# Kernel optimization log

Hardware: AMD Instinct MI355X
Metric: run time of the kernel (lower is better)

## Reference

```python
import jax, jax.numpy as jnp
import numpy as np

N = 100000
E = 1600000
D = 64  # in = hidden = out channels


def setup_inputs() -> dict:
    key = jax.random.key(0)
    ks = jax.random.split(key, 6)
    x = jax.random.normal(ks[0], (N, D), dtype=jnp.float32)
    edge_index = jax.random.randint(ks[1], (2, E), 0, N, dtype=jnp.int64)
    # bias-free linear weights, torch Linear layout [out, in]
    s = 1.0 / np.sqrt(D)
    W0 = jax.random.uniform(ks[2], (D, D), jnp.float32, -s, s)
    W1 = jax.random.uniform(ks[3], (D, D), jnp.float32, -s, s)
    Wm = jax.random.uniform(ks[4], (D, D), jnp.float32, -s, s)
    eps0 = jnp.zeros((), jnp.float32)  # train_eps=True, init 0.0
    eps1 = jnp.zeros((), jnp.float32)
    return {"x": x, "edge_index": edge_index, "W0": W0, "eps0": eps0,
            "W1": W1, "eps1": eps1, "Wm": Wm}


def reference(x, edge_index, W0, eps0, W1, eps1, Wm):
    n = x.shape[0]
    src, dst = edge_index[0], edge_index[1]

    def gin_conv(h, W, eps):
        # sparse adjacency sum-aggregation: out[i] = sum_{j->i} h[j]
        agg = jax.ops.segment_sum(h[src], dst, num_segments=n)
        # eps-scaled self-loop + bias-free linear
        return (agg + (1.0 + eps) * h) @ W.T

    h1 = jax.nn.relu(gin_conv(x, W0, eps0))   # xs[0], [N, D]
    h2 = jax.nn.relu(gin_conv(h1, W1, eps1))  # xs[1], [N, D]
    return (h1 @ Wm.T + h2) / 2.0
```

## Files before the change

### kernel.cpp

```cpp
#include <hip/hip_runtime.h>
#include <hip/hip_fp16.h>


__global__ __launch_bounds__(256) void zero_convert_kernel(
    int* __restrict__ deg, int n,
    const float* __restrict__ in, __half* __restrict__ outh, int total4)
{
    int i = blockIdx.x * blockDim.x + threadIdx.x;
    int stride = gridDim.x * blockDim.x;
    for (int k = i; k < n; k += stride) deg[k] = 0;
    const float4* in4 = (const float4*)in;
    uint2* out4 = (uint2*)outh;
    for (int k = i; k < total4; k += stride) {
        float4 v = in4[k];
        __half2 a = __floats2half2_rn(v.x, v.y);
        __half2 b = __floats2half2_rn(v.z, v.w);
        uint2 u;
        u.x = __builtin_bit_cast(unsigned int, a);
        u.y = __builtin_bit_cast(unsigned int, b);
        out4[k] = u;
    }
}

__global__ __launch_bounds__(256) void zero_int_kernel(int* __restrict__ p, int n)
{
    int i = blockIdx.x * blockDim.x + threadIdx.x;
    int stride = gridDim.x * blockDim.x;
    for (; i < n; i += stride) p[i] = 0;
}

__global__ __launch_bounds__(256) void hist_rank_kernel(
    const int* __restrict__ dst, int* __restrict__ deg,
    int* __restrict__ rank, int E)
{
    int base = (blockIdx.x * blockDim.x + threadIdx.x) * 16;
    if (base + 15 < E) {
        int4 a = *(const int4*)&dst[base];
        int4 b = *(const int4*)&dst[base + 4];
        int4 c = *(const int4*)&dst[base + 8];
        int4 d = *(const int4*)&dst[base + 12];
        int r0 = atomicAdd(&deg[a.x], 1);
        int r1 = atomicAdd(&deg[a.y], 1);
        int r2 = atomicAdd(&deg[a.z], 1);
        int r3 = atomicAdd(&deg[a.w], 1);
        int r4 = atomicAdd(&deg[b.x], 1);
        int r5 = atomicAdd(&deg[b.y], 1);
        int r6 = atomicAdd(&deg[b.z], 1);
        int r7 = atomicAdd(&deg[b.w], 1);
        int r8 = atomicAdd(&deg[c.x], 1);
        int r9 = atomicAdd(&deg[c.y], 1);
        int rA = atomicAdd(&deg[c.z], 1);
        int rB = atomicAdd(&deg[c.w], 1);
        int rC = atomicAdd(&deg[d.x], 1);
        int rD = atomicAdd(&deg[d.y], 1);
        int rE = atomicAdd(&deg[d.z], 1);
        int rF = atomicAdd(&deg[d.w], 1);
        *(int4*)&rank[base]      = make_int4(r0, r1, r2, r3);
        *(int4*)&rank[base + 4]  = make_int4(r4, r5, r6, r7);
        *(int4*)&rank[base + 8]  = make_int4(r8, r9, rA, rB);
        *(int4*)&rank[base + 12] = make_int4(rC, rD, rE, rF);
    } else {
        for (int e = base; e < E; ++e) rank[e] = atomicAdd(&deg[dst[e]], 1);
    }
}

__global__ __launch_bounds__(256) void hist_kernel(
    const int* __restrict__ dst, int* __restrict__ deg, int E)
{
    int e4 = (blockIdx.x * blockDim.x + threadIdx.x) * 4;
    if (e4 + 3 < E) {
        int4 d = *(const int4*)&dst[e4];
        atomicAdd(&deg[d.x], 1);
        atomicAdd(&deg[d.y], 1);
        atomicAdd(&deg[d.z], 1);
        atomicAdd(&deg[d.w], 1);
    } else {
        for (int e = e4; e < E; ++e) atomicAdd(&deg[dst[e]], 1);
    }
}

__global__ __launch_bounds__(256) void scanA_kernel(
    const int* __restrict__ deg, int* __restrict__ off,
    int* __restrict__ bsum, int n)
{
    __shared__ int tmp[256];
    int t = threadIdx.x;
    int base = blockIdx.x * 1024 + t * 4;
    int v0 = 0, v1 = 0, v2 = 0, v3 = 0;
    if (base + 3 < n) {
        int4 q = *(const int4*)&deg[base];
        v0 = q.x; v1 = q.y; v2 = q.z; v3 = q.w;
    } else {
        if (base + 0 < n) v0 = deg[base + 0];
        if (base + 1 < n) v1 = deg[base + 1];
        if (base + 2 < n) v2 = deg[base + 2];
    }
    int tot = v0 + v1 + v2 + v3;
    tmp[t] = tot;
    __syncthreads();
    for (int d = 1; d < 256; d <<= 1) {
        int x = (t >= d) ? tmp[t - d] : 0;
        __syncthreads();
        tmp[t] += x;
        __syncthreads();
    }
    int incl = tmp[t];
    int p = incl - tot;
    if (base + 0 < n) off[base + 0] = p;
    if (base + 1 < n) off[base + 1] = p + v0;
    if (base + 2 < n) off[base + 2] = p + v0 + v1;
    if (base + 3 < n) off[base + 3] = p + v0 + v1 + v2;
    if (t == 255) bsum[blockIdx.x] = incl;
}

__global__ __launch_bounds__(256) void scanB_kernel(int* __restrict__ bsum, int nb)
{
    __shared__ int tmp[256];
    int t = threadIdx.x;
    int v = (t < nb) ? bsum[t] : 0;
    tmp[t] = v;
    __syncthreads();
    for (int d = 1; d < 256; d <<= 1) {
        int x = (t >= d) ? tmp[t - d] : 0;
        __syncthreads();
        tmp[t] += x;
        __syncthreads();
    }
    if (t < nb) bsum[t] = tmp[t] - v;
}

__global__ __launch_bounds__(256) void scanC_kernel(
    int* __restrict__ off, int* __restrict__ cursor,
    const int* __restrict__ bsum, int n, int E)
{
    int t = threadIdx.x;
    int add = bsum[blockIdx.x];
    int base = blockIdx.x * 1024 + t * 4;
#pragma unroll
    for (int q = 0; q < 4; ++q) {
        int idx = base + q;
        if (idx < n) {
            int v = off[idx] + add;
            off[idx] = v;
            if (cursor) cursor[idx] = v;
        }
    }
    if (blockIdx.x == 0 && t == 0) off[n] = E;
}

__global__ __launch_bounds__(256) void fill_rank_kernel(
    const int* __restrict__ src, const int* __restrict__ dst,
    const int* __restrict__ rank, const int* __restrict__ off,
    int* __restrict__ bucket, int E)
{
    int base = (blockIdx.x * blockDim.x + threadIdx.x) * 8;
    if (base + 7 < E) {
        int4 d0 = *(const int4*)&dst[base];
        int4 d1 = *(const int4*)&dst[base + 4];
        int4 r0 = *(const int4*)&rank[base];
        int4 r1 = *(const int4*)&rank[base + 4];
        int4 s0 = *(const int4*)&src[base];
        int4 s1 = *(const int4*)&src[base + 4];
        bucket[off[d0.x] + r0.x] = s0.x;
        bucket[off[d0.y] + r0.y] = s0.y;
        bucket[off[d0.z] + r0.z] = s0.z;
        bucket[off[d0.w] + r0.w] = s0.w;
        bucket[off[d1.x] + r1.x] = s1.x;
        bucket[off[d1.y] + r1.y] = s1.y;
        bucket[off[d1.z] + r1.z] = s1.z;
        bucket[off[d1.w] + r1.w] = s1.w;
    } else {
        for (int e = base; e < E; ++e) bucket[off[dst[e]] + rank[e]] = src[e];
    }
}

__global__ __launch_bounds__(256) void fill_kernel(
    const int* __restrict__ src, const int* __restrict__ dst,
    int* __restrict__ cursor, int* __restrict__ bucket, int E)
{
    int e = blockIdx.x * blockDim.x + threadIdx.x;
    if (e < E) {
        int d = dst[e];
        int p = atomicAdd(&cursor[d], 1);
        bucket[p] = src[e];
    }
}

#define WPB 8

__device__ __forceinline__ __half2 bc_h2(unsigned int u)
{
    return __builtin_bit_cast(__half2, u);
}
__device__ __forceinline__ unsigned int bc_u(__half2 h)
{
    return __builtin_bit_cast(unsigned int, h);
}

#if __has_builtin(__builtin_amdgcn_fdot2)
typedef _Float16 half2_v __attribute__((ext_vector_type(2)));
__device__ __forceinline__ float fdot2(unsigned int a, unsigned int b, float c)
{
    return __builtin_amdgcn_fdot2(__builtin_bit_cast(half2_v, a),
                                  __builtin_bit_cast(half2_v, b), c, false);
}
#else
__device__ __forceinline__ float fdot2(unsigned int a, unsigned int b, float c)
{
    float2 af = __half22float2(bc_h2(a));
    float2 bf = __half22float2(bc_h2(b));
    return fmaf(af.x, bf.x, fmaf(af.y, bf.y, c));
}
#endif


__device__ __forceinline__ void xreduce4(__half2& a0, __half2& a1,
                                         __half2& a2, __half2& a3)
{
#pragma unroll
    for (int mask = 8; mask <= 32; mask <<= 1) {
        a0 = __hadd2(a0, bc_h2((unsigned int)__shfl_xor((int)bc_u(a0), mask, 64)));
        a1 = __hadd2(a1, bc_h2((unsigned int)__shfl_xor((int)bc_u(a1), mask, 64)));
        a2 = __hadd2(a2, bc_h2((unsigned int)__shfl_xor((int)bc_u(a2), mask, 64)));
        a3 = __hadd2(a3, bc_h2((unsigned int)__shfl_xor((int)bc_u(a3), mask, 64)));
    }
}

__device__ __forceinline__ void gather8(
    const __half* __restrict__ hh, const int* __restrict__ bucket,
    int beg, int end, int g, int l8,
    __half2& a0, __half2& a1, __half2& a2, __half2& a3)
{
    int j = beg;
    for (; j + 16 <= end; j += 16) {
        int sa = bucket[j + g];
        int sb = bucket[j + 8 + g];
        uint4 va = *(const uint4*)&hh[(size_t)sa * 64 + l8 * 8];
        uint4 vb = *(const uint4*)&hh[(size_t)sb * 64 + l8 * 8];
        a0 = __hadd2(__hadd2(a0, bc_h2(va.x)), bc_h2(vb.x));
        a1 = __hadd2(__hadd2(a1, bc_h2(va.y)), bc_h2(vb.y));
        a2 = __hadd2(__hadd2(a2, bc_h2(va.z)), bc_h2(vb.z));
        a3 = __hadd2(__hadd2(a3, bc_h2(va.w)), bc_h2(vb.w));
    }
    if (j + 8 <= end) {
        int sa = bucket[j + g];
        uint4 va = *(const uint4*)&hh[(size_t)sa * 64 + l8 * 8];
        a0 = __hadd2(a0, bc_h2(va.x));
        a1 = __hadd2(a1, bc_h2(va.y));
        a2 = __hadd2(a2, bc_h2(va.z));
        a3 = __hadd2(a3, bc_h2(va.w));
        j += 8;
    }
    if (j < end) {
        int jj = j + g;
        int sc = bucket[(jj < end) ? jj : (end - 1)];
        __half2 m2 = __float2half2_rn((jj < end) ? 1.0f : 0.0f);
        uint4 vc = *(const uint4*)&hh[(size_t)sc * 64 + l8 * 8];
        a0 = __hfma2(bc_h2(vc.x), m2, a0);
        a1 = __hfma2(bc_h2(vc.y), m2, a1);
        a2 = __hfma2(bc_h2(vc.z), m2, a2);
        a3 = __hfma2(bc_h2(vc.w), m2, a3);
    }
}

__global__ __launch_bounds__(512) void fused_gin_h_kernel(
    const __half* __restrict__ hh, const int* __restrict__ off,
    const int* __restrict__ bucket, const float* __restrict__ W,
    const float* __restrict__ eps, __half* __restrict__ outh, int n)
{
    __shared__ __half WhS[4096];
    __shared__ __half rowh[WPB][64];
    int tid = threadIdx.x;
    for (int idx = tid; idx < 4096; idx += 512) {
        int row = idx >> 6, col = idx & 63;
        WhS[(col >> 3) * 512 + row * 8 + (col & 7)] = __float2half(W[idx]);
    }
    __syncthreads();
    float s = 1.0f + eps[0];
    __half2 s2 = __float2half2_rn(s);
    int lane = tid & 63;
    int w = tid >> 6;
    int l8 = lane & 7;
    int g = lane >> 3;
    int wavesTotal = gridDim.x * WPB;
    const uint4* Wh4 = (const uint4*)WhS;
    for (int i = blockIdx.x * WPB + w; i < n; i += wavesTotal) {
        int2 be = *(const int2*)&off[i];
        int beg = __builtin_amdgcn_readfirstlane(be.x);
        int end = __builtin_amdgcn_readfirstlane(be.y);
        __half2 a0 = bc_h2(0u), a1 = bc_h2(0u), a2 = bc_h2(0u), a3 = bc_h2(0u);
        gather8(hh, bucket, beg, end, g, l8, a0, a1, a2, a3);
        xreduce4(a0, a1, a2, a3);
        if (g == 0) {
            uint4 sv = *(const uint4*)&hh[(size_t)i * 64 + l8 * 8];
            a0 = __hfma2(bc_h2(sv.x), s2, a0);
            a1 = __hfma2(bc_h2(sv.y), s2, a1);
            a2 = __hfma2(bc_h2(sv.z), s2, a2);
            a3 = __hfma2(bc_h2(sv.w), s2, a3);
            uint4 st;
            st.x = bc_u(a0); st.y = bc_u(a1); st.z = bc_u(a2); st.w = bc_u(a3);
            *(uint4*)&rowh[w][l8 * 8] = st;
        }
        __builtin_amdgcn_wave_barrier();
        float o = 0.f;
#pragma unroll
        for (int k4 = 0; k4 < 8; ++k4) {
            uint4 wv = Wh4[k4 * 64 + lane];
            uint4 rv = *(const uint4*)&rowh[w][k4 * 8];
            o = fdot2(wv.x, rv.x, o);
            o = fdot2(wv.y, rv.y, o);
            o = fdot2(wv.z, rv.z, o);
            o = fdot2(wv.w, rv.w, o);
        }
        outh[(size_t)i * 64 + lane] = __float2half(fmaxf(o, 0.f));
        __builtin_amdgcn_wave_barrier();
    }
}

__global__ __launch_bounds__(512) void fused_final_h_kernel(
    const __half* __restrict__ hh1, const int* __restrict__ off,
    const int* __restrict__ bucket, const float* __restrict__ W1,
    const float* __restrict__ Wm, const float* __restrict__ eps,
    float* __restrict__ out, int n)
{
    __shared__ __half W1hS[4096];
    __shared__ __half WmhS[4096];
    __shared__ __half rowh[WPB][64];
    __shared__ __half selfh[WPB][64];
    int tid = threadIdx.x;
    for (int idx = tid; idx < 4096; idx += 512) {
        int row = idx >> 6, col = idx & 63;
        int li = (col >> 3) * 512 + row * 8 + (col & 7);
        W1hS[li] = __float2half(W1[idx]);
        WmhS[li] = __float2half(Wm[idx]);
    }
    __syncthreads();
    float s = 1.0f + eps[0];
    __half2 s2 = __float2half2_rn(s);
    int lane = tid & 63;
    int w = tid >> 6;
    int l8 = lane & 7;
    int g = lane >> 3;
    int wavesTotal = gridDim.x * WPB;
    const uint4* W1h4 = (const uint4*)W1hS;
    const uint4* Wmh4 = (const uint4*)WmhS;
    for (int i = blockIdx.x * WPB + w; i < n; i += wavesTotal) {
        int2 be = *(const int2*)&off[i];
        int beg = __builtin_amdgcn_readfirstlane(be.x);
        int end = __builtin_amdgcn_readfirstlane(be.y);
        __half2 a0 = bc_h2(0u), a1 = bc_h2(0u), a2 = bc_h2(0u), a3 = bc_h2(0u);
        gather8(hh1, bucket, beg, end, g, l8, a0, a1, a2, a3);
        xreduce4(a0, a1, a2, a3);
        if (g == 0) {
            uint4 sv = *(const uint4*)&hh1[(size_t)i * 64 + l8 * 8];
            *(uint4*)&selfh[w][l8 * 8] = sv;
            a0 = __hfma2(bc_h2(sv.x), s2, a0);
            a1 = __hfma2(bc_h2(sv.y), s2, a1);
            a2 = __hfma2(bc_h2(sv.z), s2, a2);
            a3 = __hfma2(bc_h2(sv.w), s2, a3);
            uint4 st;
            st.x = bc_u(a0); st.y = bc_u(a1); st.z = bc_u(a2); st.w = bc_u(a3);
            *(uint4*)&rowh[w][l8 * 8] = st;
        }
        __builtin_amdgcn_wave_barrier();
        float o1 = 0.f, o2 = 0.f;
#pragma unroll
        for (int k4 = 0; k4 < 8; ++k4) {
            uint4 wv1 = W1h4[k4 * 64 + lane];
            uint4 wv2 = Wmh4[k4 * 64 + lane];
            uint4 rv  = *(const uint4*)&rowh[w][k4 * 8];
            uint4 sv  = *(const uint4*)&selfh[w][k4 * 8];
            o1 = fdot2(wv1.x, rv.x, o1);
            o1 = fdot2(wv1.y, rv.y, o1);
            o1 = fdot2(wv1.z, rv.z, o1);
            o1 = fdot2(wv1.w, rv.w, o1);
            o2 = fdot2(wv2.x, sv.x, o2);
            o2 = fdot2(wv2.y, sv.y, o2);
            o2 = fdot2(wv2.z, sv.z, o2);
            o2 = fdot2(wv2.w, sv.w, o2);
        }
        out[(size_t)i * 64 + lane] = (fmaxf(o1, 0.f) + o2) * 0.5f;
        __builtin_amdgcn_wave_barrier();
    }
}

__device__ __forceinline__ float dot4(float4 a, float4 b)
{
    return a.x * b.x + a.y * b.y + a.z * b.z + a.w * b.w;
}

__device__ __forceinline__ float4 gather_row_f32(
    const float* __restrict__ h, const int* __restrict__ bucket,
    int beg, int end, int g, int l16, float4 acc4)
{
    int j = beg;
    for (; j + 8 <= end; j += 8) {
        int sa = bucket[j + g];
        int sb = bucket[j + 4 + g];
        float4 va = *(const float4*)&h[(size_t)sa * 64 + l16 * 4];
        float4 vb = *(const float4*)&h[(size_t)sb * 64 + l16 * 4];
        acc4.x += va.x + vb.x;
        acc4.y += va.y + vb.y;
        acc4.z += va.z + vb.z;
        acc4.w += va.w + vb.w;
    }
    if (j + 4 <= end) {
        int sa = bucket[j + g];
        float4 va = *(const float4*)&h[(size_t)sa * 64 + l16 * 4];
        acc4.x += va.x; acc4.y += va.y; acc4.z += va.z; acc4.w += va.w;
        j += 4;
    }
    if (j < end) {
        int jj = j + g;
        int sc = bucket[(jj < end) ? jj : (end - 1)];
        float m = (jj < end) ? 1.0f : 0.0f;
        float4 vc = *(const float4*)&h[(size_t)sc * 64 + l16 * 4];
        acc4.x = fmaf(vc.x, m, acc4.x);
        acc4.y = fmaf(vc.y, m, acc4.y);
        acc4.z = fmaf(vc.z, m, acc4.z);
        acc4.w = fmaf(vc.w, m, acc4.w);
    }
    return acc4;
}

__global__ __launch_bounds__(512) void fused_gin_kernel(
    const float* __restrict__ h, const int* __restrict__ off,
    const int* __restrict__ bucket, const float* __restrict__ W,
    const float* __restrict__ eps, float* __restrict__ out, int n)
{
    __shared__ float Ws[64][68];
    __shared__ float P[WPB][4][64];
    __shared__ float rowbuf[WPB][64];
    int tid = threadIdx.x;
    for (int idx = tid; idx < 4096; idx += 512) Ws[idx >> 6][idx & 63] = W[idx];
    __syncthreads();
    float s = 1.0f + eps[0];
    int lane = tid & 63;
    int w = tid >> 6;
    int l16 = lane & 15;
    int g = lane >> 4;
    int wavesTotal = gridDim.x * WPB;
    for (int i = blockIdx.x * WPB + w; i < n; i += wavesTotal) {
        float4 init = make_float4(0.f, 0.f, 0.f, 0.f);
        if (g == 0) {
            float4 self4 = *(const float4*)&h[(size_t)i * 64 + l16 * 4];
            init = make_float4(s * self4.x, s * self4.y, s * self4.z, s * self4.w);
        }
        int2 be = *(const int2*)&off[i];
        int beg = __builtin_amdgcn_readfirstlane(be.x);
        int end = __builtin_amdgcn_readfirstlane(be.y);
        float4 acc4 = gather_row_f32(h, bucket, beg, end, g, l16, init);
        *(float4*)&P[w][g][l16 * 4] = acc4;
        __builtin_amdgcn_wave_barrier();
        float r0 = P[w][0][lane], r1 = P[w][1][lane];
        float r2 = P[w][2][lane], r3 = P[w][3][lane];
        rowbuf[w][lane] = (r0 + r1) + (r2 + r3);
        __builtin_amdgcn_wave_barrier();
        const float4* wrow = (const float4*)&Ws[lane][0];
        const float4* rrow = (const float4*)&rowbuf[w][0];
        float o = 0.f;
#pragma unroll
        for (int k4 = 0; k4 < 16; ++k4) o += dot4(wrow[k4], rrow[k4]);
        out[(size_t)i * 64 + lane] = fmaxf(o, 0.f);
        __builtin_amdgcn_wave_barrier();
    }
}

__global__ __launch_bounds__(512) void fused_final_csr_kernel(
    const float* __restrict__ h1, const int* __restrict__ off,
    const int* __restrict__ bucket, const float* __restrict__ W1,
    const float* __restrict__ Wm, const float* __restrict__ eps,
    float* __restrict__ out, int n)
{
    __shared__ float W1s[64][68];
    __shared__ float Wms[64][68];
    __shared__ float P[WPB][4][64];
    __shared__ float rowbuf[WPB][64];
    __shared__ float selfbuf[WPB][64];
    int tid = threadIdx.x;
    for (int idx = tid; idx < 4096; idx += 512) {
        W1s[idx >> 6][idx & 63] = W1[idx];
        Wms[idx >> 6][idx & 63] = Wm[idx];
    }
    __syncthreads();
    float s = 1.0f + eps[0];
    int lane = tid & 63;
    int w = tid >> 6;
    int l16 = lane & 15;
    int g = lane >> 4;
    int wavesTotal = gridDim.x * WPB;
    for (int i = blockIdx.x * WPB + w; i < n; i += wavesTotal) {
        float4 init = make_float4(0.f, 0.f, 0.f, 0.f);
        if (g == 0) {
            float4 self4 = *(const float4*)&h1[(size_t)i * 64 + l16 * 4];
            *(float4*)&selfbuf[w][l16 * 4] = self4;
            init = make_float4(s * self4.x, s * self4.y, s * self4.z, s * self4.w);
        }
        int2 be = *(const int2*)&off[i];
        int beg = __builtin_amdgcn_readfirstlane(be.x);
        int end = __builtin_amdgcn_readfirstlane(be.y);
        float4 acc4 = gather_row_f32(h1, bucket, beg, end, g, l16, init);
        *(float4*)&P[w][g][l16 * 4] = acc4;
        __builtin_amdgcn_wave_barrier();
        float r0 = P[w][0][lane], r1 = P[w][1][lane];
        float r2 = P[w][2][lane], r3 = P[w][3][lane];
        rowbuf[w][lane] = (r0 + r1) + (r2 + r3);
        __builtin_amdgcn_wave_barrier();
        const float4* w1row = (const float4*)&W1s[lane][0];
        const float4* wmrow = (const float4*)&Wms[lane][0];
        const float4* rrow  = (const float4*)&rowbuf[w][0];
        const float4* srow  = (const float4*)&selfbuf[w][0];
        float o1 = 0.f, o2 = 0.f;
#pragma unroll
        for (int k4 = 0; k4 < 16; ++k4) {
            o1 += dot4(w1row[k4], rrow[k4]);
            o2 += dot4(wmrow[k4], srow[k4]);
        }
        out[(size_t)i * 64 + lane] = (fmaxf(o1, 0.f) + o2) * 0.5f;
        __builtin_amdgcn_wave_barrier();
    }
}

__global__ __launch_bounds__(256) void init_scale_kernel(
    const float* __restrict__ h, const float* __restrict__ eps,
    float* __restrict__ agg, int total4)
{
    float s = 1.0f + eps[0];
    int i = blockIdx.x * blockDim.x + threadIdx.x;
    int stride = gridDim.x * blockDim.x;
    const float4* h4 = (const float4*)h;
    float4* a4 = (float4*)agg;
    for (; i < total4; i += stride) {
        float4 v = h4[i];
        v.x *= s; v.y *= s; v.z *= s; v.w *= s;
        a4[i] = v;
    }
}

__global__ __launch_bounds__(256) void scatter_kernel(
    const float* __restrict__ h, const int* __restrict__ src,
    const int* __restrict__ dst, float* __restrict__ agg, int E)
{
    int lane = threadIdx.x & 63;
    int e = blockIdx.x * 4 + (threadIdx.x >> 6);
    if (e >= E) return;
    int s = src[e];
    int d = dst[e];
    atomicAdd(&agg[(size_t)d * 64 + lane], h[(size_t)s * 64 + lane]);
}

__global__ __launch_bounds__(256) void gemm_relu_kernel(
    const float* __restrict__ A, const float* __restrict__ W,
    float* __restrict__ out, int n)
{
    __shared__ float Wt[64][65];
    __shared__ float rowbuf[4][64];
    int tid = threadIdx.x;
    for (int i = tid; i < 4096; i += 256) Wt[i & 63][i >> 6] = W[i];
    __syncthreads();
    int lane = tid & 63;
    int w = tid >> 6;
    int wavesTotal = gridDim.x * 4;
    for (int i = blockIdx.x * 4 + w; i < n; i += wavesTotal) {
        rowbuf[w][lane] = A[(size_t)i * 64 + lane];
        __builtin_amdgcn_wave_barrier();
        float o = 0.f;
#pragma unroll
        for (int k = 0; k < 64; ++k) o += rowbuf[w][k] * Wt[k][lane];
        out[(size_t)i * 64 + lane] = fmaxf(o, 0.f);
        __builtin_amdgcn_wave_barrier();
    }
}

__global__ __launch_bounds__(256) void final_kernel(
    const float* __restrict__ Agg, const float* __restrict__ H1,
    const float* __restrict__ W1, const float* __restrict__ Wm,
    float* __restrict__ out, int n)
{
    __shared__ float W1t[64][65];
    __shared__ float Wmt[64][65];
    __shared__ float rowbuf[4][64];
    __shared__ float selfbuf[4][64];
    int tid = threadIdx.x;
    for (int i = tid; i < 4096; i += 256) {
        W1t[i & 63][i >> 6] = W1[i];
        Wmt[i & 63][i >> 6] = Wm[i];
    }
    __syncthreads();
    int lane = tid & 63;
    int w = tid >> 6;
    int wavesTotal = gridDim.x * 4;
    for (int i = blockIdx.x * 4 + w; i < n; i += wavesTotal) {
        rowbuf[w][lane] = Agg[(size_t)i * 64 + lane];
        selfbuf[w][lane] = H1[(size_t)i * 64 + lane];
        __builtin_amdgcn_wave_barrier();
        float o1 = 0.f, o2 = 0.f;
#pragma unroll
        for (int k = 0; k < 64; ++k) {
            o1 += rowbuf[w][k] * W1t[k][lane];
            o2 += selfbuf[w][k] * Wmt[k][lane];
        }
        out[(size_t)i * 64 + lane] = (fmaxf(o1, 0.f) + o2) * 0.5f;
        __builtin_amdgcn_wave_barrier();
    }
}

extern "C" void kernel_launch(void* const* d_in, const int* in_sizes, int n_in,
                              void* d_out, int out_size, void* d_ws, size_t ws_size,
                              hipStream_t stream)
{
    const float* x    = (const float*)d_in[0];
    const int*   ei   = (const int*)d_in[1];
    const float* W0   = (const float*)d_in[2];
    const float* eps0 = (const float*)d_in[3];
    const float* W1   = (const float*)d_in[4];
    const float* eps1 = (const float*)d_in[5];
    const float* Wm   = (const float*)d_in[6];
    float* out = (float*)d_out;

    int n = in_sizes[0] / 64;
    int E = in_sizes[1] / 2;
    const int* src = ei;
    const int* dst = ei + E;

    auto align1k = [](size_t v) { return (v + 1023) & ~(size_t)1023; };

    size_t hhx_off    = 0;
    size_t hh1_off    = align1k(hhx_off + (size_t)n * 64 * 2);
    size_t off_off    = align1k(hh1_off + (size_t)n * 64 * 2);
    size_t deg_off    = align1k(off_off + (size_t)(n + 1) * 4);
    size_t bsum_off   = align1k(deg_off + (size_t)n * 4);
    size_t bucket_off = align1k(bsum_off + 256 * 4);
    size_t rank_off   = align1k(bucket_off + (size_t)(E + 64) * 4);
    size_t need_A2    = rank_off + (size_t)E * 4;

    size_t b_h1_off     = 0;
    size_t b_off_off    = align1k(b_h1_off + (size_t)n * 64 * 4);
    size_t b_deg_off    = align1k(b_off_off + (size_t)(n + 1) * 4);
    size_t b_cursor_off = align1k(b_deg_off + (size_t)n * 4);
    size_t b_bsum_off   = align1k(b_cursor_off + (size_t)n * 4);
    size_t b_bucket_off = align1k(b_bsum_off + 256 * 4);
    size_t need_B       = b_bucket_off + (size_t)E * 4;

    int nb = (n + 1023) / 1024;
    int e8Blocks  = (E + 2047) / 2048;
    int e16Blocks = (E + 4095) / 4096;
    int total4 = n * 16;

    if (ws_size >= need_A2) {
        __half* hhx  = (__half*)((char*)d_ws + hhx_off);
        __half* hh1  = (__half*)((char*)d_ws + hh1_off);
        int* off     = (int*)((char*)d_ws + off_off);
        int* deg     = (int*)((char*)d_ws + deg_off);
        int* bsum    = (int*)((char*)d_ws + bsum_off);
        int* bucket  = (int*)((char*)d_ws + bucket_off);
        int* rank    = (int*)((char*)d_ws + rank_off);

        zero_convert_kernel<<<2048, 256, 0, stream>>>(deg, n, x, hhx, total4);
        hist_rank_kernel<<<e16Blocks, 256, 0, stream>>>(dst, deg, rank, E);
        scanA_kernel<<<nb, 256, 0, stream>>>(deg, off, bsum, n);
        scanB_kernel<<<1, 256, 0, stream>>>(bsum, nb);
        scanC_kernel<<<nb, 256, 0, stream>>>(off, (int*)nullptr, bsum, n, E);
        fill_rank_kernel<<<e8Blocks, 256, 0, stream>>>(src, dst, rank, off, bucket, E);

        fused_gin_h_kernel<<<2048, 512, 0, stream>>>(hhx, off, bucket, W0, eps0, hh1, n);
        fused_final_h_kernel<<<2048, 512, 0, stream>>>(hh1, off, bucket, W1, Wm, eps1, out, n);
    } else if (ws_size >= need_B) {
        float* h1    = (float*)((char*)d_ws + b_h1_off);
        int* off     = (int*)((char*)d_ws + b_off_off);
        int* deg     = (int*)((char*)d_ws + b_deg_off);
        int* cursor  = (int*)((char*)d_ws + b_cursor_off);
        int* bsum    = (int*)((char*)d_ws + b_bsum_off);
        int* bucket  = (int*)((char*)d_ws + b_bucket_off);

        zero_int_kernel<<<256, 256, 0, stream>>>(deg, n);
        hist_kernel<<<(E + 1023) / 1024, 256, 0, stream>>>(dst, deg, E);
        scanA_kernel<<<nb, 256, 0, stream>>>(deg, off, bsum, n);
        scanB_kernel<<<1, 256, 0, stream>>>(bsum, nb);
        scanC_kernel<<<nb, 256, 0, stream>>>(off, cursor, bsum, n, E);
        fill_kernel<<<(E + 255) / 256, 256, 0, stream>>>(src, dst, cursor, bucket, E);

        fused_gin_kernel<<<1024, 512, 0, stream>>>(x, off, bucket, W0, eps0, h1, n);
        fused_final_csr_kernel<<<768, 512, 0, stream>>>(h1, off, bucket, W1, Wm, eps1, out, n);
    } else {
        float* agg = (float*)d_ws;
        float* h1  = out;
        int scatterBlocks = (E + 3) / 4;

        init_scale_kernel<<<2048, 256, 0, stream>>>(x, eps0, agg, total4);
        scatter_kernel<<<scatterBlocks, 256, 0, stream>>>(x, src, dst, agg, E);
        gemm_relu_kernel<<<2048, 256, 0, stream>>>(agg, W0, h1, n);
        init_scale_kernel<<<2048, 256, 0, stream>>>(h1, eps1, agg, total4);
        scatter_kernel<<<scatterBlocks, 256, 0, stream>>>(h1, src, dst, agg, E);
        final_kernel<<<2048, 256, 0, stream>>>(agg, h1, W1, Wm, out, n);
    }
}
```

Baseline: 219.8 us.

## Partition degree histogram into 8 copies and store edge ranks as 16-bit

The degree histogram is split into 8 per-partition count arrays, chosen by block index, so the atomics on popular destinations are spread across copies. A per-node pass turns the partition counts into per-partition prefix offsets, and a second pass adds the global CSR offset. Ranks are stored as 16-bit values to halve that traffic. The cost is two extra node-level kernels, more memory to zero, and an assumption that no per-partition degree exceeds 65535.

```diff
diff --git a/kernel.cpp b/kernel.cpp
--- a/kernel.cpp
+++ b/kernel.cpp
@@ -2,13 +2,17 @@
 #include <hip/hip_fp16.h>
 
 
+#define HIST_EPT 16
+#define HIST_EPB 4096
+#define NPART 8
+
 __global__ __launch_bounds__(256) void zero_convert_kernel(
-    int* __restrict__ deg, int n,
+    int* __restrict__ cnt, int cntTotal,
     const float* __restrict__ in, __half* __restrict__ outh, int total4)
 {
     int i = blockIdx.x * blockDim.x + threadIdx.x;
     int stride = gridDim.x * blockDim.x;
-    for (int k = i; k < n; k += stride) deg[k] = 0;
+    for (int k = i; k < cntTotal; k += stride) cnt[k] = 0;
     const float4* in4 = (const float4*)in;
     uint2* out4 = (uint2*)outh;
     for (int k = i; k < total4; k += stride) {
@@ -29,54 +33,75 @@
     for (; i < n; i += stride) p[i] = 0;
 }
 
-__global__ __launch_bounds__(256) void hist_rank_kernel(
-    const int* __restrict__ dst, int* __restrict__ deg,
-    int* __restrict__ rank, int E)
-{
-    int base = (blockIdx.x * blockDim.x + threadIdx.x) * 16;
-    if (base + 15 < E) {
+__global__ __launch_bounds__(256) void hist_rank_part_kernel(
+    const int* __restrict__ dst, int* __restrict__ cnt,
+    unsigned short* __restrict__ rank16, int E, int n)
+{
+    int b = blockIdx.x;
+    int* cp = cnt + (size_t)(b & (NPART - 1)) * n;
+    int base = b * HIST_EPB + threadIdx.x * HIST_EPT;
+    if (base + HIST_EPT - 1 < E) {
         int4 a = *(const int4*)&dst[base];
-        int4 b = *(const int4*)&dst[base + 4];
+        int4 bb = *(const int4*)&dst[base + 4];
         int4 c = *(const int4*)&dst[base + 8];
         int4 d = *(const int4*)&dst[base + 12];
-        int r0 = atomicAdd(&deg[a.x], 1);
-        int r1 = atomicAdd(&deg[a.y], 1);
-        int r2 = atomicAdd(&deg[a.z], 1);
-        int r3 = atomicAdd(&deg[a.w], 1);
-        int r4 = atomicAdd(&deg[b.x], 1);
-        int r5 = atomicAdd(&deg[b.y], 1);
-        int r6 = atomicAdd(&deg[b.z], 1);
-        int r7 = atomicAdd(&deg[b.w], 1);
-        int r8 = atomicAdd(&deg[c.x], 1);
-        int r9 = atomicAdd(&deg[c.y], 1);
-        int rA = atomicAdd(&deg[c.z], 1);
-        int rB = atomicAdd(&deg[c.w], 1);
-        int rC = atomicAdd(&deg[d.x], 1);
-        int rD = atomicAdd(&deg[d.y], 1);
-        int rE = atomicAdd(&deg[d.z], 1);
-        int rF = atomicAdd(&deg[d.w], 1);
-        *(int4*)&rank[base]      = make_int4(r0, r1, r2, r3);
-        *(int4*)&rank[base + 4]  = make_int4(r4, r5, r6, r7);
-        *(int4*)&rank[base + 8]  = make_int4(r8, r9, rA, rB);
-        *(int4*)&rank[base + 12] = make_int4(rC, rD, rE, rF);
+        unsigned int r0 = (unsigned int)atomicAdd(&cp[a.x], 1);
+        unsigned int r1 = (unsigned int)atomicAdd(&cp[a.y], 1);
+        unsigned int r2 = (unsigned int)atomicAdd(&cp[a.z], 1);
+        unsigned int r3 = (unsigned int)atomicAdd(&cp[a.w], 1);
+        unsigned int r4 = (unsigned int)atomicAdd(&cp[bb.x], 1);
+        unsigned int r5 = (unsigned int)atomicAdd(&cp[bb.y], 1);
+        unsigned int r6 = (unsigned int)atomicAdd(&cp[bb.z], 1);
+        unsigned int r7 = (unsigned int)atomicAdd(&cp[bb.w], 1);
+        unsigned int r8 = (unsigned int)atomicAdd(&cp[c.x], 1);
+        unsigned int r9 = (unsigned int)atomicAdd(&cp[c.y], 1);
+        unsigned int rA = (unsigned int)atomicAdd(&cp[c.z], 1);
+        unsigned int rB = (unsigned int)atomicAdd(&cp[c.w], 1);
+        unsigned int rC = (unsigned int)atomicAdd(&cp[d.x], 1);
+        unsigned int rD = (unsigned int)atomicAdd(&cp[d.y], 1);
+        unsigned int rE = (unsigned int)atomicAdd(&cp[d.z], 1);
+        unsigned int rF = (unsigned int)atomicAdd(&cp[d.w], 1);
+        uint4 w0, w1;
+        w0.x = (r1 << 16) | (r0 & 0xffffu);
+        w0.y = (r3 << 16) | (r2 & 0xffffu);
+        w0.z = (r5 << 16) | (r4 & 0xffffu);
+        w0.w = (r7 << 16) | (r6 & 0xffffu);
+        w1.x = (r9 << 16) | (r8 & 0xffffu);
+        w1.y = (rB << 16) | (rA & 0xffffu);
+        w1.z = (rD << 16) | (rC & 0xffffu);
+        w1.w = (rF << 16) | (rE & 0xffffu);
+        *(uint4*)&rank16[base] = w0;
+        *(uint4*)&rank16[base + 8] = w1;
     } else {
-        for (int e = base; e < E; ++e) rank[e] = atomicAdd(&deg[dst[e]], 1);
-    }
-}
-
-__global__ __launch_bounds__(256) void hist_kernel(
-    const int* __restrict__ dst, int* __restrict__ deg, int E)
-{
-    int e4 = (blockIdx.x * blockDim.x + threadIdx.x) * 4;
-    if (e4 + 3 < E) {
-        int4 d = *(const int4*)&dst[e4];
-        atomicAdd(&deg[d.x], 1);
-        atomicAdd(&deg[d.y], 1);
-        atomicAdd(&deg[d.z], 1);
-        atomicAdd(&deg[d.w], 1);
-    } else {
-        for (int e = e4; e < E; ++e) atomicAdd(&deg[dst[e]], 1);
-    }
+        for (int e = base; e < E; ++e)
+            rank16[e] = (unsigned short)atomicAdd(&cp[dst[e]], 1);
+    }
+}
+
+__global__ __launch_bounds__(256) void reduce_poff_kernel(
+    int* __restrict__ cnt, int* __restrict__ deg, int n)
+{
+    int d = blockIdx.x * blockDim.x + threadIdx.x;
+    if (d >= n) return;
+    int run = 0;
+#pragma unroll
+    for (int p = 0; p < NPART; ++p) {
+        size_t idx = (size_t)p * n + d;
+        int t = cnt[idx];
+        cnt[idx] = run;
+        run += t;
+    }
+    deg[d] = run;
+}
+
+__global__ __launch_bounds__(256) void addoff_kernel(
+    int* __restrict__ cnt, const int* __restrict__ off, int n)
+{
+    int d = blockIdx.x * blockDim.x + threadIdx.x;
+    if (d >= n) return;
+    int o = off[d];
+#pragma unroll
+    for (int p = 0; p < NPART; ++p) cnt[(size_t)p * n + d] += o;
 }
 
 __global__ __launch_bounds__(256) void scanA_kernel(
@@ -148,29 +173,47 @@
     if (blockIdx.x == 0 && t == 0) off[n] = E;
 }
 
-__global__ __launch_bounds__(256) void fill_rank_kernel(
+__global__ __launch_bounds__(256) void fill_rank_part_kernel(
     const int* __restrict__ src, const int* __restrict__ dst,
-    const int* __restrict__ rank, const int* __restrict__ off,
-    int* __restrict__ bucket, int E)
+    const unsigned short* __restrict__ rank16, const int* __restrict__ cnt,
+    int* __restrict__ bucket, int E, int n)
 {
     int base = (blockIdx.x * blockDim.x + threadIdx.x) * 8;
     if (base + 7 < E) {
+        const int* cp = cnt + (size_t)((base >> 12) & (NPART - 1)) * n;
         int4 d0 = *(const int4*)&dst[base];
         int4 d1 = *(const int4*)&dst[base + 4];
-        int4 r0 = *(const int4*)&rank[base];
-        int4 r1 = *(const int4*)&rank[base + 4];
+        uint4 r = *(const uint4*)&rank16[base];
         int4 s0 = *(const int4*)&src[base];
         int4 s1 = *(const int4*)&src[base + 4];
-        bucket[off[d0.x] + r0.x] = s0.x;
-        bucket[off[d0.y] + r0.y] = s0.y;
-        bucket[off[d0.z] + r0.z] = s0.z;
-        bucket[off[d0.w] + r0.w] = s0.w;
-        bucket[off[d1.x] + r1.x] = s1.x;
-        bucket[off[d1.y] + r1.y] = s1.y;
-        bucket[off[d1.z] + r1.z] = s1.z;
-        bucket[off[d1.w] + r1.w] = s1.w;
+        bucket[cp[d0.x] + (int)(r.x & 0xffffu)] = s0.x;
+        bucket[cp[d0.y] + (int)(r.x >> 16)]     = s0.y;
+        bucket[cp[d0.z] + (int)(r.y & 0xffffu)] = s0.z;
+        bucket[cp[d0.w] + (int)(r.y >> 16)]     = s0.w;
+        bucket[cp[d1.x] + (int)(r.z & 0xffffu)] = s1.x;
+        bucket[cp[d1.y] + (int)(r.z >> 16)]     = s1.y;
+        bucket[cp[d1.z] + (int)(r.w & 0xffffu)] = s1.z;
+        bucket[cp[d1.w] + (int)(r.w >> 16)]     = s1.w;
     } else {
-        for (int e = base; e < E; ++e) bucket[off[dst[e]] + rank[e]] = src[e];
+        for (int e = base; e < E; ++e) {
+            const int* cp = cnt + (size_t)((e >> 12) & (NPART - 1)) * n;
+            bucket[cp[dst[e]] + (int)rank16[e]] = src[e];
+        }
+    }
+}
+
+__global__ __launch_bounds__(256) void hist_kernel(
+    const int* __restrict__ dst, int* __restrict__ deg, int E)
+{
+    int e4 = (blockIdx.x * blockDim.x + threadIdx.x) * 4;
+    if (e4 + 3 < E) {
+        int4 d = *(const int4*)&dst[e4];
+        atomicAdd(&deg[d.x], 1);
+        atomicAdd(&deg[d.y], 1);
+        atomicAdd(&deg[d.z], 1);
+        atomicAdd(&deg[d.w], 1);
+    } else {
+        for (int e = e4; e < E; ++e) atomicAdd(&deg[dst[e]], 1);
     }
 }
 
@@ -212,7 +255,6 @@
     return fmaf(af.x, bf.x, fmaf(af.y, bf.y, c));
 }
 #endif
-
 
 __device__ __forceinline__ void xreduce4(__half2& a0, __half2& a1,
                                          __half2& a2, __half2& a3)
@@ -630,9 +672,10 @@
     size_t off_off    = align1k(hh1_off + (size_t)n * 64 * 2);
     size_t deg_off    = align1k(off_off + (size_t)(n + 1) * 4);
     size_t bsum_off   = align1k(deg_off + (size_t)n * 4);
-    size_t bucket_off = align1k(bsum_off + 256 * 4);
-    size_t rank_off   = align1k(bucket_off + (size_t)(E + 64) * 4);
-    size_t need_A2    = rank_off + (size_t)E * 4;
+    size_t cnt_off    = align1k(bsum_off + 256 * 4);
+    size_t bucket_off = align1k(cnt_off + (size_t)NPART * n * 4);
+    size_t rank_off   = align1k(bucket_off + (size_t)E * 4);
+    size_t need_A2    = rank_off + (size_t)E * 2;
 
     size_t b_h1_off     = 0;
     size_t b_off_off    = align1k(b_h1_off + (size_t)n * 64 * 4);
@@ -643,8 +686,9 @@
     size_t need_B       = b_bucket_off + (size_t)E * 4;
 
     int nb = (n + 1023) / 1024;
-    int e8Blocks  = (E + 2047) / 2048;
-    int e16Blocks = (E + 4095) / 4096;
+    int histBlocks = (E + HIST_EPB - 1) / HIST_EPB;
+    int nodeBlocks = (n + 255) / 256;
+    int fillBlocks = (E + 2047) / 2048;
     int total4 = n * 16;
 
     if (ws_size >= need_A2) {
@@ -653,15 +697,18 @@
         int* off     = (int*)((char*)d_ws + off_off);
         int* deg     = (int*)((char*)d_ws + deg_off);
         int* bsum    = (int*)((char*)d_ws + bsum_off);
+        int* cnt     = (int*)((char*)d_ws + cnt_off);
         int* bucket  = (int*)((char*)d_ws + bucket_off);
-        int* rank    = (int*)((char*)d_ws + rank_off);
-
-        zero_convert_kernel<<<2048, 256, 0, stream>>>(deg, n, x, hhx, total4);
-        hist_rank_kernel<<<e16Blocks, 256, 0, stream>>>(dst, deg, rank, E);
+        unsigned short* rank16 = (unsigned short*)((char*)d_ws + rank_off);
+
+        zero_convert_kernel<<<2048, 256, 0, stream>>>(cnt, NPART * n, x, hhx, total4);
+        hist_rank_part_kernel<<<histBlocks, 256, 0, stream>>>(dst, cnt, rank16, E, n);
+        reduce_poff_kernel<<<nodeBlocks, 256, 0, stream>>>(cnt, deg, n);
         scanA_kernel<<<nb, 256, 0, stream>>>(deg, off, bsum, n);
         scanB_kernel<<<1, 256, 0, stream>>>(bsum, nb);
         scanC_kernel<<<nb, 256, 0, stream>>>(off, (int*)nullptr, bsum, n, E);
-        fill_rank_kernel<<<e8Blocks, 256, 0, stream>>>(src, dst, rank, off, bucket, E);
+        addoff_kernel<<<nodeBlocks, 256, 0, stream>>>(cnt, off, n);
+        fill_rank_part_kernel<<<fillBlocks, 256, 0, stream>>>(src, dst, rank16, cnt, bucket, E, n);
 
         fused_gin_h_kernel<<<2048, 512, 0, stream>>>(hhx, off, bucket, W0, eps0, hh1, n);
         fused_final_h_kernel<<<2048, 512, 0, stream>>>(hh1, off, bucket, W1, Wm, eps1, out, n);
```

Result: no change. 222.0 us (+1.0%).
